# Performance work log

Hardware: AMD Instinct MI355X
Metric: run time of the kernel (lower is better)

The kernel has to match this reference:

```python
import jax, jax.numpy as jnp
import numpy as np

EPS = 1e-8  # smoothing_radius


def setup_inputs() -> dict:
    key = jax.random.key(0)
    ks = jax.random.split(key, 8)
    T, S, D = 2048, 1024, 3
    H, FIN, FOUT = 64, 7, 4
    return {
        "reference_length": jnp.ones((), jnp.float32),
        "source_points": jax.random.normal(ks[0], (S, D), jnp.float32),
        "target_points": jax.random.normal(ks[1], (T, D), jnp.float32),
        "source_strengths": jax.random.uniform(ks[2], (S,), jnp.float32),
        "source_area": jax.random.uniform(ks[3], (S,), jnp.float32),
        "source_normal": jax.random.normal(ks[4], (S, D), jnp.float32),
        "W1": jax.random.normal(ks[5], (FIN, H), jnp.float32) / np.sqrt(FIN),
        "b1": jnp.zeros((H,), jnp.float32),
        "W2": jax.random.normal(ks[6], (H, FOUT), jnp.float32) / np.sqrt(H),
        "b2": jnp.zeros((FOUT,), jnp.float32),
    }


def _legendre4(x):
    # First 4 Legendre polynomials P1..P4 (n_spherical_harmonics = 4)
    x2 = x * x
    p1 = x
    p2 = 0.5 * (3.0 * x2 - 1.0)
    p3 = 0.5 * (5.0 * x2 - 3.0) * x
    p4 = 0.125 * ((35.0 * x2 - 30.0) * x2 + 3.0)
    return jnp.stack([p1, p2, p3, p4], axis=-1)


def _kernel_forward(reference_length, source_points, target_points,
                    source_strengths, source_area, source_normal,
                    W1, b1, W2, b2):
    D = source_points.shape[-1]
    # Dimensionless relative positions: [T, S, D]
    r = (target_points[:, None, :] - source_points[None, :, :]) / reference_length
    r2 = jnp.sum(r * r, axis=-1) + EPS * EPS          # [T, S]
    n2 = jnp.sum(source_normal * source_normal, -1) + EPS * EPS  # [S]
    # Invariant features: source scalar, smoothed log-magnitudes, pair Legendre terms
    log_r = 0.5 * jnp.log(r2)                          # [T, S]
    log_n = 0.5 * jnp.log(n2)                          # [S]
    cos = jnp.einsum('tsd,sd->ts', r, source_normal) / jnp.sqrt(r2 * n2[None, :])
    feats = jnp.concatenate([
        jnp.broadcast_to(source_area[None, :, None], r2.shape + (1,)),
        log_r[..., None],
        jnp.broadcast_to(log_n[None, :, None], r2.shape + (1,)),
        _legendre4(cos),
    ], axis=-1)                                        # [T, S, 7]
    # MLP kernel network with tanh squashing (network_type='mlp')
    h = jax.nn.silu(feats @ W1 + b1)                   # [T, S, 64]
    out = jnp.tanh(h @ W2 + b2)                        # [T, S, 4]
    # Physical far-field decay: scalar ~ 1/r^{D-2}, vector ~ 1/r^{D-1}
    inv_r = jax.lax.rsqrt(r2)
    decay_s = inv_r ** (D - 2)
    decay_v = inv_r ** (D - 1)
    w = source_strengths[None, :]                      # [1, S]
    scalar = jnp.sum(w * decay_s * out[..., 0], axis=-1)  # [T]
    # Rotationally invariant vector reprojection: radial + 2 coeffs per non-radial vector
    r_hat = r * inv_r[..., None]
    n_hat = source_normal / jnp.sqrt(n2)[:, None]
    n_hat_b = jnp.broadcast_to(n_hat[None], r.shape)
    vec = (out[..., 1:2] * r_hat
           + out[..., 2:3] * n_hat_b
           + out[..., 3:4] * jnp.cross(r_hat, n_hat_b))  # [T, S, D]
    vector = jnp.einsum('ts,tsd->td', w * decay_v, vec)   # [T, D]
    return jnp.concatenate([scalar[:, None], vector], axis=-1)  # [T, 1+D]


def reference(reference_length, source_points, target_points, source_strengths,
              source_area, source_normal, W1, b1, W2, b2):
    return _kernel_forward(reference_length, source_points, target_points,
                           source_strengths, source_area, source_normal,
                           W1, b1, W2, b2)
```

## Files before the change

### kernel.cpp

```cpp
#include <hip/hip_runtime.h>

typedef float v2f __attribute__((ext_vector_type(2)));

#define EPS2 1e-16f

constexpr int H      = 64;
constexpr int PBLOCK = 256;
constexpr int BLOCK  = 512;
constexpr int NCHUNK = 2;
constexpr float LOG2E = 1.4426950408889634f;

__device__ __forceinline__ float rcpf_fast(float x) { return __builtin_amdgcn_rcpf(x); }
__device__ __forceinline__ float rsqf_fast(float x) { return __builtin_amdgcn_rsqf(x); }
__device__ __forceinline__ float exp2_fast(float x) { return __builtin_amdgcn_exp2f(x); }
__device__ __forceinline__ v2f splat(float x) { return v2f{x, x}; }
__device__ __forceinline__ v2f vfma(v2f a, v2f b, v2f c) { return __builtin_elementwise_fma(a, b, c); }

__global__ void prep(const float* __restrict__ refLenP,
                     const float* __restrict__ srcP,
                     const float* __restrict__ srcN,
                     const float* __restrict__ wgtP,
                     const float* __restrict__ areaP,
                     const float* __restrict__ W1,
                     const float* __restrict__ b1,
                     const float* __restrict__ W2,
                     float* __restrict__ ws, int S)
{
    const int nSrcBlk = (S + PBLOCK - 1) / PBLOCK;
    const int bid = blockIdx.x;
    if (bid < nSrcBlk) {
        const int s = bid * PBLOCK + threadIdx.x;
        if (s < S) {
            const float invL = rcpf_fast(refLenP[0]);
            float px = srcP[s * 3 + 0] * invL;
            float py = srcP[s * 3 + 1] * invL;
            float pz = srcP[s * 3 + 2] * invL;
            float nx = srcN[s * 3 + 0];
            float ny = srcN[s * 3 + 1];
            float nz = srcN[s * 3 + 2];
            float n2 = fmaf(nx, nx, fmaf(ny, ny, nz * nz)) + EPS2;
            float inv_n = rsqf_fast(n2);
            float l2n = __log2f(n2);
            float4* sPA = (float4*)(ws + 1024);
            float4* sNB = (float4*)(ws + 1024 + 4 * S);
            float*  sw  = ws + 1024 + 8 * S;
            sPA[s] = make_float4(px, py, pz, areaP[s]);
            sNB[s] = make_float4(nx * inv_n, ny * inv_n, nz * inv_n, l2n);
            sw[s]  = wgtP[s];
        }
    } else {
        const int h = threadIdx.x;
        if (h < H) {
            float* p = ws + h * 16;
            p[0] = -LOG2E * W1[0 * H + h];
            p[1] = -0.5f  * W1[1 * H + h];
            p[2] = -0.5f  * W1[2 * H + h];
            p[3] = -LOG2E * W1[3 * H + h];
            p[4] = -LOG2E * W1[4 * H + h];
            p[5] = -LOG2E * W1[5 * H + h];
            p[6] = -LOG2E * W1[6 * H + h];
            p[7] = -LOG2E * b1[h];
            p[8]  = -2.0f * W2[h * 4 + 0];
            p[9]  = -2.0f * W2[h * 4 + 1];
            p[10] = -2.0f * W2[h * 4 + 2];
            p[11] = -2.0f * W2[h * 4 + 3];
            p[12] = 0.f; p[13] = 0.f; p[14] = 0.f; p[15] = 0.f;
        }
    }
}

__global__ __launch_bounds__(BLOCK, 8)
void bh_kernel(const float* __restrict__ refLenP,
               const float* __restrict__ tgtP,
               const float* __restrict__ b2,
               const float* __restrict__ ws,
               float* __restrict__ out,
               int S, int T)
{
    __shared__ float red[8][8];

    const int tid = threadIdx.x;
    const int t0 = blockIdx.x * 2;
    const int t1 = t0 + 1;
    const bool has1 = (t1 < T);
    const int t1c = has1 ? t1 : t0;

    const float invL = rcpf_fast(refLenP[0]);
    const v2f txv = v2f{tgtP[t0 * 3 + 0] * invL, tgtP[t1c * 3 + 0] * invL};
    const v2f tyv = v2f{tgtP[t0 * 3 + 1] * invL, tgtP[t1c * 3 + 1] * invL};
    const v2f tzv = v2f{tgtP[t0 * 3 + 2] * invL, tgtP[t1c * 3 + 2] * invL};

    const float4* __restrict__ sPA = (const float4*)(ws + 1024);
    const float4* __restrict__ sNB = (const float4*)(ws + 1024 + 4 * S);
    const float*  __restrict__ sw  = ws + 1024 + 8 * S;
    const float4* __restrict__ wq  = (const float4*)ws;

    v2f f1[NCHUNK], f3[NCHUNK], f4[NCHUNK], f5[NCHUNK], f6[NCHUNK];
    float fa[NCHUNK], f2s[NCHUNK];
    #pragma unroll
    for (int c = 0; c < NCHUNK; ++c) {
        const int s = tid + c * BLOCK;
        const int sc = (s < S) ? s : (S - 1);
        const float4 pa = sPA[sc];
        const float4 nb = sNB[sc];
        v2f rx = txv - splat(pa.x);
        v2f ry = tyv - splat(pa.y);
        v2f rz = tzv - splat(pa.z);
        v2f r2 = vfma(rx, rx, vfma(ry, ry, vfma(rz, rz, splat(EPS2))));
        v2f ir = v2f{rsqf_fast(r2.x), rsqf_fast(r2.y)};
        f1[c] = v2f{__log2f(r2.x), __log2f(r2.y)};
        v2f cosv = vfma(rx, splat(nb.x), vfma(ry, splat(nb.y), rz * splat(nb.z))) * ir;
        v2f c2 = cosv * cosv;
        fa[c]  = pa.w;
        f2s[c] = nb.w;
        f3[c] = cosv;
        f4[c] = vfma(c2, splat(1.5f), splat(-0.5f));
        f5[c] = (c2 * splat(2.5f) - splat(1.5f)) * cosv;
        f6[c] = vfma(vfma(c2, splat(4.375f), splat(-3.75f)), c2, splat(0.375f));
    }

    v2f o0[NCHUNK], o1[NCHUNK], o2[NCHUNK], o3[NCHUNK];
    {
        const float s2 = 2.0f * LOG2E;
        const float b20 = s2 * b2[0], b21 = s2 * b2[1];
        const float b22 = s2 * b2[2], b23 = s2 * b2[3];
        #pragma unroll
        for (int c = 0; c < NCHUNK; ++c) {
            o0[c] = splat(b20); o1[c] = splat(b21);
            o2[c] = splat(b22); o3[c] = splat(b23);
        }
    }

    #pragma unroll 4
    for (int h = 0; h < H; ++h) {
        const float4 wa = wq[h * 4 + 0];
        const float4 wb = wq[h * 4 + 1];
        const float4 w2 = wq[h * 4 + 2];
        #pragma unroll
        for (int c = 0; c < NCHUNK; ++c) {
            float abase = fmaf(fa[c], wa.x, fmaf(f2s[c], wa.z, wb.w));
            v2f a = vfma(f1[c], splat(wa.y), splat(abase));
            a = vfma(f3[c], splat(wa.w), a);
            a = vfma(f4[c], splat(wb.x), a);
            a = vfma(f5[c], splat(wb.y), a);
            a = vfma(f6[c], splat(wb.z), a);
            v2f e  = v2f{exp2_fast(a.x), exp2_fast(a.y)};
            v2f sg = v2f{rcpf_fast(1.0f + e.x), rcpf_fast(1.0f + e.y)};
            v2f hv = a * sg;
            o0[c] = vfma(hv, splat(w2.x), o0[c]);
            o1[c] = vfma(hv, splat(w2.y), o1[c]);
            o2[c] = vfma(hv, splat(w2.z), o2[c]);
            o3[c] = vfma(hv, splat(w2.w), o3[c]);
        }
    }

    v2f a0 = splat(0.f), a1 = splat(0.f), a2 = splat(0.f), a3 = splat(0.f);
    #pragma unroll
    for (int c = 0; c < NCHUNK; ++c) {
        const int s = tid + c * BLOCK;
        const int sc = (s < S) ? s : (S - 1);
        const float4 pa = sPA[sc];
        const float4 nb = sNB[sc];
        const float wgt = (s < S) ? sw[sc] : 0.0f;
        v2f rx = txv - splat(pa.x);
        v2f ry = tyv - splat(pa.y);
        v2f rz = tzv - splat(pa.z);
        v2f r2 = vfma(rx, rx, vfma(ry, ry, vfma(rz, rz, splat(EPS2))));
        v2f ir = v2f{rsqf_fast(r2.x), rsqf_fast(r2.y)};
        v2f wsv = splat(wgt) * ir;
        v2f wvv = wsv * ir;

        v2f tt[4];
        v2f oo[4] = {o0[c], o1[c], o2[c], o3[c]};
        #pragma unroll
        for (int k = 0; k < 4; ++k) {
            v2f m = __builtin_elementwise_min(__builtin_elementwise_max(oo[k], splat(-126.f)), splat(126.f));
            v2f E = v2f{exp2_fast(m.x), exp2_fast(m.y)};
            v2f num = E - splat(1.0f);
            v2f den = v2f{rcpf_fast(E.x + 1.0f), rcpf_fast(E.y + 1.0f)};
            tt[k] = num * den;
        }

        a0 = vfma(wsv, tt[0], a0);
        v2f rhx = rx * ir, rhy = ry * ir, rhz = rz * ir;
        v2f cxx = rhy * splat(nb.z) - rhz * splat(nb.y);
        v2f cxy = rhz * splat(nb.x) - rhx * splat(nb.z);
        v2f cxz = rhx * splat(nb.y) - rhy * splat(nb.x);
        v2f vx = tt[1] * rhx + tt[2] * splat(nb.x) + tt[3] * cxx;
        v2f vy = tt[1] * rhy + tt[2] * splat(nb.y) + tt[3] * cxy;
        v2f vz = tt[1] * rhz + tt[2] * splat(nb.z) + tt[3] * cxz;
        a1 = vfma(wvv, vx, a1);
        a2 = vfma(wvv, vy, a2);
        a3 = vfma(wvv, vz, a3);
    }

    float r8[8] = {a0.x, a1.x, a2.x, a3.x, a0.y, a1.y, a2.y, a3.y};
    #pragma unroll
    for (int off = 32; off > 0; off >>= 1) {
        #pragma unroll
        for (int k = 0; k < 8; ++k) r8[k] += __shfl_down(r8[k], off);
    }
    const int wave = tid >> 6;
    const int lane = tid & 63;
    if (lane == 0) {
        #pragma unroll
        for (int k = 0; k < 8; ++k) red[wave][k] = r8[k];
    }
    __syncthreads();
    if (tid < 8) {
        float v = 0.0f;
        #pragma unroll
        for (int w = 0; w < 8; ++w) v += red[w][tid];
        if (tid < 4) out[t0 * 4 + tid] = v;
        else if (has1) out[t1 * 4 + (tid - 4)] = v;
    }
}

extern "C" void kernel_launch(void* const* d_in, const int* in_sizes, int n_in,
                              void* d_out, int out_size, void* d_ws, size_t ws_size,
                              hipStream_t stream) {
    const float* refLen = (const float*)d_in[0];
    const float* srcP   = (const float*)d_in[1];
    const float* tgtP   = (const float*)d_in[2];
    const float* w      = (const float*)d_in[3];
    const float* area   = (const float*)d_in[4];
    const float* srcN   = (const float*)d_in[5];
    const float* W1     = (const float*)d_in[6];
    const float* b1     = (const float*)d_in[7];
    const float* W2     = (const float*)d_in[8];
    const float* b2     = (const float*)d_in[9];
    float* out          = (float*)d_out;
    float* ws           = (float*)d_ws;

    const int S = in_sizes[3];
    const int T = in_sizes[2] / 3;
    const int nSrcBlk = (S + PBLOCK - 1) / PBLOCK;
    const int nTgtBlk = (T + 1) / 2;

    prep<<<nSrcBlk + 1, PBLOCK, 0, stream>>>(refLen, srcP, srcN, w, area, W1, b1, W2, ws, S);
    bh_kernel<<<nTgtBlk, BLOCK, 0, stream>>>(refLen, tgtP, b2, ws, out, S, T);
}
```

Baseline: 120.5 us.

## Drop packed two-target v2f math for scalar one-target-per-block mapping

Each block now handles a single target with 256 threads, and each thread covers 4 sources in scalar float instead of 2 sources times 2 targets in packed v2f. The W1 layout swaps the bias and last-weight slots to match the new FMA chain, and launch_bounds occupancy hinting is removed. This gives up packed-FMA throughput (v_pk_fma) for more blocks and simpler per-thread work. Transcendental cost per pair is unchanged, so the MLP inner loop may lose ALU efficiency on the FMA part.

```diff
diff --git a/kernel.cpp b/kernel.cpp
--- a/kernel.cpp
+++ b/kernel.cpp
@@ -1,20 +1,16 @@
 #include <hip/hip_runtime.h>
-
-typedef float v2f __attribute__((ext_vector_type(2)));
 
 #define EPS2 1e-16f
 
 constexpr int H      = 64;
 constexpr int PBLOCK = 256;
-constexpr int BLOCK  = 512;
-constexpr int NCHUNK = 2;
+constexpr int BLOCK  = 256;
+constexpr int NCHUNK = 4;
 constexpr float LOG2E = 1.4426950408889634f;
 
 __device__ __forceinline__ float rcpf_fast(float x) { return __builtin_amdgcn_rcpf(x); }
 __device__ __forceinline__ float rsqf_fast(float x) { return __builtin_amdgcn_rsqf(x); }
 __device__ __forceinline__ float exp2_fast(float x) { return __builtin_amdgcn_exp2f(x); }
-__device__ __forceinline__ v2f splat(float x) { return v2f{x, x}; }
-__device__ __forceinline__ v2f vfma(v2f a, v2f b, v2f c) { return __builtin_elementwise_fma(a, b, c); }
 
 __global__ void prep(const float* __restrict__ refLenP,
                      const float* __restrict__ srcP,
@@ -58,8 +54,8 @@
             p[3] = -LOG2E * W1[3 * H + h];
             p[4] = -LOG2E * W1[4 * H + h];
             p[5] = -LOG2E * W1[5 * H + h];
-            p[6] = -LOG2E * W1[6 * H + h];
-            p[7] = -LOG2E * b1[h];
+            p[6] = -LOG2E * b1[h];
+            p[7] = -LOG2E * W1[6 * H + h];
             p[8]  = -2.0f * W2[h * 4 + 0];
             p[9]  = -2.0f * W2[h * 4 + 1];
             p[10] = -2.0f * W2[h * 4 + 2];
@@ -69,7 +65,7 @@
     }
 }
 
-__global__ __launch_bounds__(BLOCK, 8)
+__global__ __launch_bounds__(BLOCK)
 void bh_kernel(const float* __restrict__ refLenP,
                const float* __restrict__ tgtP,
                const float* __restrict__ b2,
@@ -77,25 +73,22 @@
                float* __restrict__ out,
                int S, int T)
 {
-    __shared__ float red[8][8];
+    __shared__ float red[4][4];
 
     const int tid = threadIdx.x;
-    const int t0 = blockIdx.x * 2;
-    const int t1 = t0 + 1;
-    const bool has1 = (t1 < T);
-    const int t1c = has1 ? t1 : t0;
+    const int t = blockIdx.x;
 
     const float invL = rcpf_fast(refLenP[0]);
-    const v2f txv = v2f{tgtP[t0 * 3 + 0] * invL, tgtP[t1c * 3 + 0] * invL};
-    const v2f tyv = v2f{tgtP[t0 * 3 + 1] * invL, tgtP[t1c * 3 + 1] * invL};
-    const v2f tzv = v2f{tgtP[t0 * 3 + 2] * invL, tgtP[t1c * 3 + 2] * invL};
+    const float tx = tgtP[t * 3 + 0] * invL;
+    const float ty = tgtP[t * 3 + 1] * invL;
+    const float tz = tgtP[t * 3 + 2] * invL;
 
     const float4* __restrict__ sPA = (const float4*)(ws + 1024);
     const float4* __restrict__ sNB = (const float4*)(ws + 1024 + 4 * S);
     const float*  __restrict__ sw  = ws + 1024 + 8 * S;
     const float4* __restrict__ wq  = (const float4*)ws;
 
-    v2f f1[NCHUNK], f3[NCHUNK], f4[NCHUNK], f5[NCHUNK], f6[NCHUNK];
+    float f1[NCHUNK], f3[NCHUNK], f4[NCHUNK], f5[NCHUNK], f6[NCHUNK];
     float fa[NCHUNK], f2s[NCHUNK];
     #pragma unroll
     for (int c = 0; c < NCHUNK; ++c) {
@@ -103,31 +96,30 @@
         const int sc = (s < S) ? s : (S - 1);
         const float4 pa = sPA[sc];
         const float4 nb = sNB[sc];
-        v2f rx = txv - splat(pa.x);
-        v2f ry = tyv - splat(pa.y);
-        v2f rz = tzv - splat(pa.z);
-        v2f r2 = vfma(rx, rx, vfma(ry, ry, vfma(rz, rz, splat(EPS2))));
-        v2f ir = v2f{rsqf_fast(r2.x), rsqf_fast(r2.y)};
-        f1[c] = v2f{__log2f(r2.x), __log2f(r2.y)};
-        v2f cosv = vfma(rx, splat(nb.x), vfma(ry, splat(nb.y), rz * splat(nb.z))) * ir;
-        v2f c2 = cosv * cosv;
+        float rx = tx - pa.x;
+        float ry = ty - pa.y;
+        float rz = tz - pa.z;
+        float r2 = fmaf(rx, rx, fmaf(ry, ry, fmaf(rz, rz, EPS2)));
+        float ir = rsqf_fast(r2);
+        f1[c] = __log2f(r2);
+        float cosv = fmaf(rx, nb.x, fmaf(ry, nb.y, rz * nb.z)) * ir;
+        float c2 = cosv * cosv;
         fa[c]  = pa.w;
         f2s[c] = nb.w;
         f3[c] = cosv;
-        f4[c] = vfma(c2, splat(1.5f), splat(-0.5f));
-        f5[c] = (c2 * splat(2.5f) - splat(1.5f)) * cosv;
-        f6[c] = vfma(vfma(c2, splat(4.375f), splat(-3.75f)), c2, splat(0.375f));
-    }
-
-    v2f o0[NCHUNK], o1[NCHUNK], o2[NCHUNK], o3[NCHUNK];
+        f4[c] = fmaf(c2, 1.5f, -0.5f);
+        f5[c] = (c2 * 2.5f - 1.5f) * cosv;
+        f6[c] = fmaf(fmaf(c2, 4.375f, -3.75f), c2, 0.375f);
+    }
+
+    float o0[NCHUNK], o1[NCHUNK], o2[NCHUNK], o3[NCHUNK];
     {
         const float s2 = 2.0f * LOG2E;
         const float b20 = s2 * b2[0], b21 = s2 * b2[1];
         const float b22 = s2 * b2[2], b23 = s2 * b2[3];
         #pragma unroll
         for (int c = 0; c < NCHUNK; ++c) {
-            o0[c] = splat(b20); o1[c] = splat(b21);
-            o2[c] = splat(b22); o3[c] = splat(b23);
+            o0[c] = b20; o1[c] = b21; o2[c] = b22; o3[c] = b23;
         }
     }
 
@@ -138,23 +130,23 @@
         const float4 w2 = wq[h * 4 + 2];
         #pragma unroll
         for (int c = 0; c < NCHUNK; ++c) {
-            float abase = fmaf(fa[c], wa.x, fmaf(f2s[c], wa.z, wb.w));
-            v2f a = vfma(f1[c], splat(wa.y), splat(abase));
-            a = vfma(f3[c], splat(wa.w), a);
-            a = vfma(f4[c], splat(wb.x), a);
-            a = vfma(f5[c], splat(wb.y), a);
-            a = vfma(f6[c], splat(wb.z), a);
-            v2f e  = v2f{exp2_fast(a.x), exp2_fast(a.y)};
-            v2f sg = v2f{rcpf_fast(1.0f + e.x), rcpf_fast(1.0f + e.y)};
-            v2f hv = a * sg;
-            o0[c] = vfma(hv, splat(w2.x), o0[c]);
-            o1[c] = vfma(hv, splat(w2.y), o1[c]);
-            o2[c] = vfma(hv, splat(w2.z), o2[c]);
-            o3[c] = vfma(hv, splat(w2.w), o3[c]);
-        }
-    }
-
-    v2f a0 = splat(0.f), a1 = splat(0.f), a2 = splat(0.f), a3 = splat(0.f);
+            float a = fmaf(fa[c], wa.x, fmaf(f2s[c], wa.z, wb.z));
+            a = fmaf(f1[c], wa.y, a);
+            a = fmaf(f3[c], wa.w, a);
+            a = fmaf(f4[c], wb.x, a);
+            a = fmaf(f5[c], wb.y, a);
+            a = fmaf(f6[c], wb.w, a);
+            float e  = exp2_fast(a);
+            float sg = rcpf_fast(1.0f + e);
+            float hv = a * sg;
+            o0[c] = fmaf(hv, w2.x, o0[c]);
+            o1[c] = fmaf(hv, w2.y, o1[c]);
+            o2[c] = fmaf(hv, w2.z, o2[c]);
+            o3[c] = fmaf(hv, w2.w, o3[c]);
+        }
+    }
+
+    float acc0 = 0.f, acc1 = 0.f, acc2 = 0.f, acc3 = 0.f;
     #pragma unroll
     for (int c = 0; c < NCHUNK; ++c) {
         const int s = tid + c * BLOCK;
@@ -162,57 +154,53 @@
         const float4 pa = sPA[sc];
         const float4 nb = sNB[sc];
         const float wgt = (s < S) ? sw[sc] : 0.0f;
-        v2f rx = txv - splat(pa.x);
-        v2f ry = tyv - splat(pa.y);
-        v2f rz = tzv - splat(pa.z);
-        v2f r2 = vfma(rx, rx, vfma(ry, ry, vfma(rz, rz, splat(EPS2))));
-        v2f ir = v2f{rsqf_fast(r2.x), rsqf_fast(r2.y)};
-        v2f wsv = splat(wgt) * ir;
-        v2f wvv = wsv * ir;
-
-        v2f tt[4];
-        v2f oo[4] = {o0[c], o1[c], o2[c], o3[c]};
+        float rx = tx - pa.x;
+        float ry = ty - pa.y;
+        float rz = tz - pa.z;
+        float r2 = fmaf(rx, rx, fmaf(ry, ry, fmaf(rz, rz, EPS2)));
+        float ir = rsqf_fast(r2);
+        float wsv = wgt * ir;
+        float wvv = wsv * ir;
+
+        float tt[4];
+        float oo[4] = {o0[c], o1[c], o2[c], o3[c]};
         #pragma unroll
         for (int k = 0; k < 4; ++k) {
-            v2f m = __builtin_elementwise_min(__builtin_elementwise_max(oo[k], splat(-126.f)), splat(126.f));
-            v2f E = v2f{exp2_fast(m.x), exp2_fast(m.y)};
-            v2f num = E - splat(1.0f);
-            v2f den = v2f{rcpf_fast(E.x + 1.0f), rcpf_fast(E.y + 1.0f)};
-            tt[k] = num * den;
-        }
-
-        a0 = vfma(wsv, tt[0], a0);
-        v2f rhx = rx * ir, rhy = ry * ir, rhz = rz * ir;
-        v2f cxx = rhy * splat(nb.z) - rhz * splat(nb.y);
-        v2f cxy = rhz * splat(nb.x) - rhx * splat(nb.z);
-        v2f cxz = rhx * splat(nb.y) - rhy * splat(nb.x);
-        v2f vx = tt[1] * rhx + tt[2] * splat(nb.x) + tt[3] * cxx;
-        v2f vy = tt[1] * rhy + tt[2] * splat(nb.y) + tt[3] * cxy;
-        v2f vz = tt[1] * rhz + tt[2] * splat(nb.z) + tt[3] * cxz;
-        a1 = vfma(wvv, vx, a1);
-        a2 = vfma(wvv, vy, a2);
-        a3 = vfma(wvv, vz, a3);
-    }
-
-    float r8[8] = {a0.x, a1.x, a2.x, a3.x, a0.y, a1.y, a2.y, a3.y};
+            float m = fminf(fmaxf(oo[k], -126.f), 126.f);
+            float E = exp2_fast(m);
+            tt[k] = (E - 1.0f) * rcpf_fast(E + 1.0f);
+        }
+
+        acc0 = fmaf(wsv, tt[0], acc0);
+        float rhx = rx * ir, rhy = ry * ir, rhz = rz * ir;
+        float cxx = rhy * nb.z - rhz * nb.y;
+        float cxy = rhz * nb.x - rhx * nb.z;
+        float cxz = rhx * nb.y - rhy * nb.x;
+        float vx = tt[1] * rhx + tt[2] * nb.x + tt[3] * cxx;
+        float vy = tt[1] * rhy + tt[2] * nb.y + tt[3] * cxy;
+        float vz = tt[1] * rhz + tt[2] * nb.z + tt[3] * cxz;
+        acc1 = fmaf(wvv, vx, acc1);
+        acc2 = fmaf(wvv, vy, acc2);
+        acc3 = fmaf(wvv, vz, acc3);
+    }
+
     #pragma unroll
     for (int off = 32; off > 0; off >>= 1) {
-        #pragma unroll
-        for (int k = 0; k < 8; ++k) r8[k] += __shfl_down(r8[k], off);
+        acc0 += __shfl_down(acc0, off);
+        acc1 += __shfl_down(acc1, off);
+        acc2 += __shfl_down(acc2, off);
+        acc3 += __shfl_down(acc3, off);
     }
     const int wave = tid >> 6;
     const int lane = tid & 63;
     if (lane == 0) {
-        #pragma unroll
-        for (int k = 0; k < 8; ++k) red[wave][k] = r8[k];
+        red[wave][0] = acc0; red[wave][1] = acc1;
+        red[wave][2] = acc2; red[wave][3] = acc3;
     }
     __syncthreads();
-    if (tid < 8) {
-        float v = 0.0f;
-        #pragma unroll
-        for (int w = 0; w < 8; ++w) v += red[w][tid];
-        if (tid < 4) out[t0 * 4 + tid] = v;
-        else if (has1) out[t1 * 4 + (tid - 4)] = v;
+    if (tid < 4) {
+        float v = red[0][tid] + red[1][tid] + red[2][tid] + red[3][tid];
+        out[t * 4 + tid] = v;
     }
 }
 
@@ -235,8 +223,7 @@
     const int S = in_sizes[3];
     const int T = in_sizes[2] / 3;
     const int nSrcBlk = (S + PBLOCK - 1) / PBLOCK;
-    const int nTgtBlk = (T + 1) / 2;
 
     prep<<<nSrcBlk + 1, PBLOCK, 0, stream>>>(refLen, srcP, srcN, w, area, W1, b1, W2, ws, S);
-    bh_kernel<<<nTgtBlk, BLOCK, 0, stream>>>(refLen, tgtP, b2, ws, out, S, T);
+    bh_kernel<<<T, BLOCK, 0, stream>>>(refLen, tgtP, b2, ws, out, S, T);
 }
```

Result: no change. 120.7 us (+0.2%).
